# Performance work log

Hardware: AMD Instinct MI355X
Metric: run time of the kernel (lower is better)

## Reference

```python
import jax, jax.numpy as jnp
import numpy as np

N = 4096      # mesh nodes (seq len)
D = 512       # input_dim_nodes / hidden_size
F = 512       # ffn_hidden_size (hidden_dim)
NH = 4        # num_attention_heads
HD = D // NH  # head dim = 128
L = 2         # processor_layers
EPS = 1e-5
SCALE = 1.0 / float(np.sqrt(HD))
NEG = -1e9


def setup_inputs() -> dict:
    key = jax.random.key(0)
    ks = jax.random.split(key, 16)
    nfeat = jax.random.normal(ks[0], (N, D), jnp.float32)
    # sparse graph adjacency mask: True = masked out (TE 'arbitrary' convention)
    mask = jax.random.uniform(ks[1], (N, N)) < 0.99
    idx = jnp.arange(N)
    mask = mask.at[idx, idx].set(False)  # keep self-edges unmasked
    s = 0.02
    p = lambda k, shape: jax.random.normal(k, shape, jnp.float32) * s
    return dict(
        nfeat=nfeat, mask=mask,
        ln1_g=jnp.ones((L, D), jnp.float32), ln1_b=jnp.zeros((L, D), jnp.float32),
        wq=p(ks[2], (L, D, D)), bq=p(ks[3], (L, D)),
        wk=p(ks[4], (L, D, D)), bk=p(ks[5], (L, D)),
        wv=p(ks[6], (L, D, D)), bv=p(ks[7], (L, D)),
        wo=p(ks[8], (L, D, D)), bo=p(ks[9], (L, D)),
        ln2_g=jnp.ones((L, D), jnp.float32), ln2_b=jnp.zeros((L, D), jnp.float32),
        fc1_w=p(ks[10], (L, F, D)), fc1_b=p(ks[11], (L, F)),
        fc2_w=p(ks[12], (L, D, F)), fc2_b=p(ks[13], (L, D)),
    )


def _ln(x, g, b):
    mu = x.mean(-1, keepdims=True)
    var = ((x - mu) ** 2).mean(-1, keepdims=True)
    return (x - mu) * jax.lax.rsqrt(var + EPS) * g + b


def reference(nfeat, mask, ln1_g, ln1_b, wq, bq, wk, bk, wv, bv, wo, bo,
              ln2_g, ln2_b, fc1_w, fc1_b, fc2_w, fc2_b):
    def layer(x, p):
        g1, b1, Wq, Bq, Wk, Bk, Wv, Bv, Wo, Bo, g2, b2, W1, B1, W2, B2 = p
        # --- pre-LN self-attention with arbitrary mask ---
        h = _ln(x, g1, b1)                                  # [N, D]
        q = (h @ Wq.T + Bq).reshape(N, NH, HD)
        k = (h @ Wk.T + Bk).reshape(N, NH, HD)
        v = (h @ Wv.T + Bv).reshape(N, NH, HD)
        scores = jnp.einsum('qhd,khd->hqk', q, k) * SCALE   # [NH, N, N]
        scores = jnp.where(mask[None], NEG, scores)
        attn = jax.nn.softmax(scores, axis=-1)
        o = jnp.einsum('hqk,khd->qhd', attn, v).reshape(N, D)
        x = x + o @ Wo.T + Bo
        # --- pre-LN MLP ---
        h2 = _ln(x, g2, b2)
        m = jax.nn.gelu(h2 @ W1.T + B1, approximate=False) @ W2.T + B2
        return x + m, None

    xs = (ln1_g, ln1_b, wq, bq, wk, bk, wv, bv, wo, bo,
          ln2_g, ln2_b, fc1_w, fc1_b, fc2_w, fc2_b)
    out, _ = jax.lax.scan(layer, nfeat, xs)
    return out
```

## Files before the change

### kernel.cpp

```cpp
#include <hip/hip_runtime.h>
#include <math.h>

#define NN 4096
#define DD 512
#define FF 512
#define CAP 256
#define SCALE 0.08838834764831845f

typedef unsigned short u16;
typedef unsigned char u8;
typedef __attribute__((ext_vector_type(8))) short short8;
typedef __attribute__((ext_vector_type(8))) unsigned short ushort8;
typedef __attribute__((ext_vector_type(4))) unsigned short ushort4v;
typedef __attribute__((ext_vector_type(4))) float floatx4;
typedef __attribute__((ext_vector_type(2))) float f32x2;
typedef _Float16 half8v __attribute__((ext_vector_type(8)));

__device__ __forceinline__ float bf2f(u16 u) {
    union { unsigned int i; float f; } x; x.i = ((unsigned int)u) << 16; return x.f;
}
__device__ __forceinline__ u16 f2bf(float f) {
    union { float f; unsigned int i; } x; x.f = f;
    unsigned int r = (x.i + 0x7FFFu + ((x.i >> 16) & 1u)) >> 16;
    return (u16)r;
}
__device__ __forceinline__ u16 f2h(float f) {
    _Float16 h = (_Float16)f;
    union { _Float16 h; u16 u; } x; x.h = h; return x.u;
}
__device__ __forceinline__ u8 f2fp8(float f) {
    union { _Float16 h; u16 u; } x;
    x.h = (_Float16)(f * 0.00390625f);
    u16 h = x.u;
    h = h + 0x3F + ((h >> 7) & 1);
    return (u8)(((h >> 8) & 0x80) | ((h >> 7) & 0x7f));
}
__device__ __forceinline__ float fp82f_sw(u8 b) {
    union { u16 u; _Float16 h; } x;
    x.u = (u16)(((u16)(b & 0x80) << 8) | ((u16)(b & 0x7f) << 7));
    return (float)x.h * 256.0f;
}
__device__ __forceinline__ void gld_lds16(const void* g, void* l) {
    __builtin_amdgcn_global_load_lds((const __attribute__((address_space(1))) void*)g,
                                     (__attribute__((address_space(3))) void*)l, 16, 0, 0);
}

struct W6 {
    const float* w[6];
    const float* bq; const float* bk; const float* bv;
};
__global__ void setup_kernel(W6 wp, u16* __restrict__ dst, float* __restrict__ bcat,
                             const int* __restrict__ mask, int* __restrict__ idx,
                             int* __restrict__ cnt) {
    __shared__ int c;
    if (blockIdx.x >= 192) {
        int row = blockIdx.x - 192;
        if (threadIdx.x == 0) c = 0;
        __syncthreads();
        const int4* mrow = (const int4*)(mask + (size_t)row * NN);
        for (int j4 = threadIdx.x; j4 < NN / 4; j4 += blockDim.x) {
            int4 m4 = mrow[j4];
            int base = j4 * 4;
            if (m4.x == 0) idx[row * CAP + atomicAdd(&c, 1)] = base;
            if (m4.y == 0) idx[row * CAP + atomicAdd(&c, 1)] = base + 1;
            if (m4.z == 0) idx[row * CAP + atomicAdd(&c, 1)] = base + 2;
            if (m4.w == 0) idx[row * CAP + atomicAdd(&c, 1)] = base + 3;
        }
        __syncthreads();
        if (threadIdx.x == 0) cnt[row] = (c < CAP) ? c : CAP;
        return;
    }
    int region = blockIdx.x >> 4;
    int layer = region / 6, mat = region - layer * 6;
    const float* src = wp.w[mat] + (size_t)layer * (DD * DD);
    u16* d = dst + (size_t)region * (DD * DD);
    int off = (blockIdx.x & 15) * 16384 + threadIdx.x * 4;
#pragma unroll
    for (int i = 0; i < 16; i++) {
        int e = off + i * 1024;
        float4 f = *(const float4*)&src[e];
        ushort4v u;
        u.x = f2bf(f.x); u.y = f2bf(f.y); u.z = f2bf(f.z); u.w = f2bf(f.w);
        *(ushort4v*)&d[e] = u;
    }
    if (blockIdx.x < 2) {
        int l = blockIdx.x;
        for (int it = 0; it < 6; it++) {
            int j = it * 256 + threadIdx.x;
            int m = j >> 9, col = j & 511;
            const float* bp = (m == 0) ? wp.bq : (m == 1) ? wp.bk : wp.bv;
            bcat[l * 1536 + j] = bp[l * DD + col];
        }
    }
}

__global__ void ln_kernel(const float* __restrict__ x, const float* __restrict__ g,
                          const float* __restrict__ b, u16* __restrict__ out) {
    int wave = threadIdx.x >> 6, lane = threadIdx.x & 63;
    int row = blockIdx.x * 4 + wave;
    const float* xr = x + (size_t)row * DD;
    float4 p0 = *(const float4*)&xr[lane * 8];
    float4 p1 = *(const float4*)&xr[lane * 8 + 4];
    float v[8] = {p0.x, p0.y, p0.z, p0.w, p1.x, p1.y, p1.z, p1.w};
    float s = 0.f;
#pragma unroll
    for (int i = 0; i < 8; i++) s += v[i];
#pragma unroll
    for (int off = 32; off; off >>= 1) s += __shfl_xor(s, off);
    float mu = s * (1.0f / DD);
    float vs = 0.f;
#pragma unroll
    for (int i = 0; i < 8; i++) { float d = v[i] - mu; vs += d * d; }
#pragma unroll
    for (int off = 32; off; off >>= 1) vs += __shfl_xor(vs, off);
    float r = rsqrtf(vs * (1.0f / DD) + 1e-5f);
    float4 g0 = *(const float4*)&g[lane * 8];
    float4 g1 = *(const float4*)&g[lane * 8 + 4];
    float4 b0 = *(const float4*)&b[lane * 8];
    float4 b1 = *(const float4*)&b[lane * 8 + 4];
    float ge[8] = {g0.x, g0.y, g0.z, g0.w, g1.x, g1.y, g1.z, g1.w};
    float be[8] = {b0.x, b0.y, b0.z, b0.w, b1.x, b1.y, b1.z, b1.w};
    ushort8 ov;
#pragma unroll
    for (int i = 0; i < 8; i++) ov[i] = f2bf((v[i] - mu) * r * ge[i] + be[i]);
    *(ushort8*)&out[(size_t)row * DD + lane * 8] = ov;
}

__device__ __forceinline__ float gelu_fast(float val) {
    float z = fabsf(val) * 0.70710678118654752f;
    float tt = __builtin_amdgcn_rcpf(fmaf(0.3275911f, z, 1.0f));
    float p = fmaf(1.061405429f, tt, -1.453152027f);
    p = fmaf(p, tt, 1.421413741f);
    p = fmaf(p, tt, -0.284496736f);
    p = fmaf(p, tt, 0.254829592f);
    p = p * tt * __expf(-z * z);
    float er_ = 1.0f - p;
    float sgn = (val < 0.f) ? -er_ : er_;
    return val * 0.5f * (1.0f + sgn);
}


template <int MODE>
__launch_bounds__(256)
__global__ void gemm_bf16(const u16* __restrict__ A, const u16* __restrict__ B,
                          const float* __restrict__ bias, const float* __restrict__ resIn,
                          float* __restrict__ resOut, u16* __restrict__ outB,
                          int M, int Nout, int K) {
    __shared__ u16 As[2 * 64 * 64];
    __shared__ u16 Bs[2 * 64 * 64];
    const int m0 = blockIdx.y * 64, n0 = blockIdx.x * 64;
    const int t = threadIdx.x;
    const int wave = t >> 6, lane = t & 63;
    const int wm = (wave & 1) * 32, wn = (wave >> 1) * 32;
    const int sr = t >> 3;
    const int sc = ((((t & 7) - (t >> 3)) & 7)) * 8;
    const int fr = lane & 15, g0 = lane >> 4;
    const int er = (lane >> 4) * 4, ec = lane & 15;

    floatx4 acc[2][2] = {};
    const u16* ag0 = A + (size_t)(m0 + sr) * K + sc;
    const u16* ag1 = A + (size_t)(m0 + 32 + sr) * K + sc;
    const u16* bg0 = B + (size_t)(n0 + sr) * K + sc;
    const u16* bg1 = B + (size_t)(n0 + 32 + sr) * K + sc;
    u16* as0 = As + t * 8;
    u16* as1 = As + 32 * 64 + t * 8;
    u16* bs0 = Bs + t * 8;
    u16* bs1 = Bs + 32 * 64 + t * 8;

    float rin[16];
    if (MODE == 2) {
#pragma unroll
        for (int i = 0; i < 2; i++)
#pragma unroll
            for (int j = 0; j < 2; j++)
#pragma unroll
                for (int r = 0; r < 4; r++)
                    rin[(i * 2 + j) * 4 + r] =
                        resIn[(size_t)(m0 + wm + 16 * i + er + r) * Nout + (n0 + wn + 16 * j + ec)];
    }

    auto stage = [&](int buf, int k0) {
        int o = buf * 4096;
        gld_lds16(ag0 + k0, as0 + o);
        gld_lds16(ag1 + k0, as1 + o);
        gld_lds16(bg0 + k0, bs0 + o);
        gld_lds16(bg1 + k0, bs1 + o);
    };

    const int NK = K >> 6;
    stage(0, 0);
    int cur = 0;
    for (int kt = 0; kt < NK; kt++) {
        __syncthreads();
        if (kt + 1 < NK) stage(cur ^ 1, (kt + 1) * 64);
        const u16* Ab = As + cur * 4096;
        const u16* Bb = Bs + cur * 4096;
#pragma unroll
        for (int h = 0; h < 2; h++) {
            const int fo = (((h << 2) + g0 + fr) & 7) << 3;
            short8 af[2], bf[2];
#pragma unroll
            for (int i = 0; i < 2; i++) af[i] = *(const short8*)&Ab[(wm + 16 * i + fr) * 64 + fo];
#pragma unroll
            for (int j = 0; j < 2; j++) bf[j] = *(const short8*)&Bb[(wn + 16 * j + fr) * 64 + fo];
#pragma unroll
            for (int i = 0; i < 2; i++)
#pragma unroll
                for (int j = 0; j < 2; j++)
                    acc[i][j] = __builtin_amdgcn_mfma_f32_16x16x32_bf16(af[i], bf[j], acc[i][j], 0, 0, 0);
        }
        cur ^= 1;
    }

#pragma unroll
    for (int i = 0; i < 2; i++) {
#pragma unroll
        for (int j = 0; j < 2; j++) {
            int col = n0 + wn + 16 * j + ec;
            float bsv = bias[col];
#pragma unroll
            for (int r = 0; r < 4; r++) {
                int row = m0 + wm + 16 * i + er + r;
                float val = acc[i][j][r] + bsv;
                if (MODE == 1) val = gelu_fast(val);
                if (MODE == 2) {
                    resOut[(size_t)row * Nout + col] = rin[(i * 2 + j) * 4 + r] + val;
                } else {
                    outB[(size_t)row * Nout + col] = f2bf(val);
                }
            }
        }
    }
}

__launch_bounds__(256)
__global__ void gemm_qkv(const u16* __restrict__ A, const u16* __restrict__ B,
                         const float* __restrict__ bias, u16* __restrict__ qOut,
                         u8* __restrict__ kv8) {
    __shared__ u16 As[2 * 128 * 64];
    __shared__ u16 Bs[2 * 64 * 64];
    const int m0 = blockIdx.y * 128, n0 = blockIdx.x * 64;
    const int t = threadIdx.x;
    const int wave = t >> 6, lane = t & 63;
    const int wm = (wave & 1) * 64, wn = (wave >> 1) * 32;
    const int sr = t >> 3;
    const int sc = ((((t & 7) - (t >> 3)) & 7)) * 8;
    const int fr = lane & 15, g0 = lane >> 4;

    floatx4 acc[4][2] = {};
    const u16* agp[4];
    u16* asp[4];
#pragma unroll
    for (int u = 0; u < 4; u++) {
        agp[u] = A + (size_t)(m0 + 32 * u + sr) * DD + sc;
        asp[u] = As + u * (32 * 64) + t * 8;
    }
    const u16* bg0 = B + (size_t)(n0 + sr) * DD + sc;
    const u16* bg1 = B + (size_t)(n0 + 32 + sr) * DD + sc;
    u16* bs0 = Bs + t * 8;
    u16* bs1 = Bs + 32 * 64 + t * 8;

    auto stage = [&](int buf, int k0) {
        int oa = buf * 8192, ob = buf * 4096;
#pragma unroll
        for (int u = 0; u < 4; u++) gld_lds16(agp[u] + k0, asp[u] + oa);
        gld_lds16(bg0 + k0, bs0 + ob);
        gld_lds16(bg1 + k0, bs1 + ob);
    };

    stage(0, 0);
    int cur = 0;
    for (int kt = 0; kt < 8; kt++) {
        __syncthreads();
        if (kt + 1 < 8) stage(cur ^ 1, (kt + 1) * 64);
        const u16* Ab = As + cur * 8192;
        const u16* Bb = Bs + cur * 4096;
#pragma unroll
        for (int h = 0; h < 2; h++) {
            const int fo = (((h << 2) + g0 + fr) & 7) << 3;
            short8 af[4], bf[2];
#pragma unroll
            for (int i = 0; i < 4; i++) af[i] = *(const short8*)&Ab[(wm + 16 * i + fr) * 64 + fo];
#pragma unroll
            for (int j = 0; j < 2; j++) bf[j] = *(const short8*)&Bb[(wn + 16 * j + fr) * 64 + fo];
#pragma unroll
            for (int i = 0; i < 4; i++)
#pragma unroll
                for (int j = 0; j < 2; j++)
                    acc[i][j] = __builtin_amdgcn_mfma_f32_16x16x32_bf16(af[i], bf[j], acc[i][j], 0, 0, 0);
        }
        cur ^= 1;
    }

    const int er = (lane >> 4) * 4, ec = lane & 15;
    const int bx = blockIdx.x;
#pragma unroll
    for (int j = 0; j < 2; j++) {
        int col = n0 + wn + 16 * j + ec;
        float bsv = bias[col];
#pragma unroll
        for (int i = 0; i < 4; i++) {
#pragma unroll
            for (int r = 0; r < 4; r++) {
                int row = m0 + wm + 16 * i + er + r;
                float val = acc[i][j][r] + bsv;
                if (bx < 8) {
                    qOut[(size_t)row * 512 + col] = f2h(val);
                } else if (bx < 16) {
                    int cc = col - 512;
                    kv8[(size_t)row * 1024 + 16 * (cc >> 3) + (cc & 7)] = f2fp8(val);
                } else {
                    int cc = col - 1024;
                    kv8[(size_t)row * 1024 + 16 * (cc >> 3) + 8 + (cc & 7)] = f2fp8(val);
                }
            }
        }
    }
}

__global__ void sparse_attn(const u16* __restrict__ q, const u8* __restrict__ kv8,
                            const int* __restrict__ idx, const int* __restrict__ cnt,
                            u16* __restrict__ o) {
    int t = threadIdx.x;
    int wave = t >> 6, lane = t & 63;
    int qslot = wave >> 1, half = wave & 1;
    int qi = blockIdx.x * 4 + qslot;
    __shared__ float obuf[4][64][8];
    __shared__ float sbuf[4][64];
    __shared__ int sidx[4][CAP];

    int c = cnt[qi];
    const int* ir = idx + qi * CAP;
    for (int j = t & 127; j < c; j += 128) sidx[qslot][j] = ir[j];

    half8v qv = *(const half8v*)(q + (size_t)qi * 512 + lane * 8);
    float qf[8];
#pragma unroll
    for (int e = 0; e < 8; e++) qf[e] = (float)qv[e];
    __syncthreads();

    float sum = 0.f, oa[8] = {};
    int j = half;
    int4 kv0, kv1;
    {
        int k0i = (j < c) ? sidx[qslot][j] : 0;
        int k1i = (j + 2 < c) ? sidx[qslot][j + 2] : 0;
        kv0 = *(const int4*)(kv8 + (size_t)k0i * 1024 + lane * 16);
        kv1 = *(const int4*)(kv8 + (size_t)k1i * 1024 + lane * 16);
    }
    while (j < c) {
        int4 kvn;
        {
            int kjn = (j + 4 < c) ? sidx[qslot][j + 4] : 0;
            kvn = *(const int4*)(kv8 + (size_t)kjn * 1024 + lane * 16);
        }
        float kd[8], vd[8];
#if __has_builtin(__builtin_amdgcn_cvt_pk_f32_fp8)
        {
            f32x2 p0 = __builtin_amdgcn_cvt_pk_f32_fp8(kv0.x, false);
            f32x2 p1 = __builtin_amdgcn_cvt_pk_f32_fp8(kv0.x, true);
            f32x2 p2 = __builtin_amdgcn_cvt_pk_f32_fp8(kv0.y, false);
            f32x2 p3 = __builtin_amdgcn_cvt_pk_f32_fp8(kv0.y, true);
            kd[0] = p0.x; kd[1] = p0.y; kd[2] = p1.x; kd[3] = p1.y;
            kd[4] = p2.x; kd[5] = p2.y; kd[6] = p3.x; kd[7] = p3.y;
            f32x2 p4 = __builtin_amdgcn_cvt_pk_f32_fp8(kv0.z, false);
            f32x2 p5 = __builtin_amdgcn_cvt_pk_f32_fp8(kv0.z, true);
            f32x2 p6 = __builtin_amdgcn_cvt_pk_f32_fp8(kv0.w, false);
            f32x2 p7 = __builtin_amdgcn_cvt_pk_f32_fp8(kv0.w, true);
            vd[0] = p4.x; vd[1] = p4.y; vd[2] = p5.x; vd[3] = p5.y;
            vd[4] = p6.x; vd[5] = p6.y; vd[6] = p7.x; vd[7] = p7.y;
        }
#else
        {
            const u8* bp = (const u8*)&kv0;
#pragma unroll
            for (int e = 0; e < 8; e++) { kd[e] = fp82f_sw(bp[e]); vd[e] = fp82f_sw(bp[8 + e]); }
        }
#endif
        float d = 0.f;
#pragma unroll
        for (int e = 0; e < 8; e++) d = fmaf(qf[e], kd[e], d);
        d += __shfl_xor(d, 1);
        d += __shfl_xor(d, 2);
        d += __shfl_xor(d, 4);
        d += __shfl_xor(d, 8);
        float p = __expf(d * SCALE);
        sum += p;
#pragma unroll
        for (int e = 0; e < 8; e++) oa[e] = fmaf(p, vd[e], oa[e]);
        kv0 = kv1;
        kv1 = kvn;
        j += 2;
    }

    if (half == 1) {
#pragma unroll
        for (int e = 0; e < 8; e++) obuf[qslot][lane][e] = oa[e];
        sbuf[qslot][lane] = sum;
    }
    __syncthreads();
    if (half == 0) {
        sum += sbuf[qslot][lane];
        float inv = 1.0f / sum;
        ushort8 ov;
#pragma unroll
        for (int e = 0; e < 8; e++) ov[e] = f2bf((oa[e] + obuf[qslot][lane][e]) * inv);
        *(ushort8*)(o + (size_t)qi * 512 + lane * 8) = ov;
    }
}

extern "C" void kernel_launch(void* const* d_in, const int* in_sizes, int n_in,
                              void* d_out, int out_size, void* d_ws, size_t ws_size,
                              hipStream_t stream) {
    const float* nfeat = (const float*)d_in[0];
    const int*   mask  = (const int*)d_in[1];
    const float* ln1_g = (const float*)d_in[2];
    const float* ln1_b = (const float*)d_in[3];
    const float* bo    = (const float*)d_in[11];
    const float* ln2_g = (const float*)d_in[12];
    const float* ln2_b = (const float*)d_in[13];
    const float* fc1_b = (const float*)d_in[15];
    const float* fc2_b = (const float*)d_in[17];

    const size_t ND = (size_t)NN * DD;
    float* x    = (float*)d_ws;
    u16*   h    = (u16*)(x + ND);
    u16*   q    = h + ND;
    u8*    kv8  = (u8*)(q + ND);
    u16*   o    = (u16*)(kv8 + (size_t)NN * 1024);
    u16*   m1   = o + ND;
    u16*   wc   = m1 + ND;
    float* bcat = (float*)(wc + (size_t)12 * DD * DD);
    int*   idx  = (int*)(bcat + 2 * 1536);
    int*   cnt  = idx + (size_t)NN * CAP;

    W6 w6;
    w6.w[0] = (const float*)d_in[4];  w6.w[1] = (const float*)d_in[6];
    w6.w[2] = (const float*)d_in[8];  w6.w[3] = (const float*)d_in[10];
    w6.w[4] = (const float*)d_in[14]; w6.w[5] = (const float*)d_in[16];
    w6.bq = (const float*)d_in[5]; w6.bk = (const float*)d_in[7]; w6.bv = (const float*)d_in[9];
    setup_kernel<<<192 + NN, 256, 0, stream>>>(w6, wc, bcat, mask, idx, cnt);

    const size_t SS = (size_t)DD * DD;
    for (int l = 0; l < 2; l++) {
        size_t bOff = (size_t)l * DD;
        u16* wl = wc + (size_t)l * 6 * SS;
        const float* xin = (l == 0) ? nfeat : x;
        float* fc2_dst = (l == 1) ? (float*)d_out : x;

        ln_kernel<<<NN / 4, 256, 0, stream>>>(xin, ln1_g + bOff, ln1_b + bOff, h);
        gemm_qkv<<<dim3(24, 32), 256, 0, stream>>>(h, wl, bcat + l * 1536, q, kv8);
        sparse_attn<<<NN / 4, 512, 0, stream>>>(q, kv8, idx, cnt, o);
        gemm_bf16<2><<<dim3(8, 64), 256, 0, stream>>>(o, wl + 3 * SS, bo + bOff,
                                                      xin, x, nullptr, NN, DD, DD);
        ln_kernel<<<NN / 4, 256, 0, stream>>>(x, ln2_g + bOff, ln2_b + bOff, h);
        gemm_bf16<1><<<dim3(8, 64), 256, 0, stream>>>(h, wl + 4 * SS, fc1_b + bOff,
                                                      nullptr, nullptr, m1, NN, FF, DD);
        gemm_bf16<2><<<dim3(8, 64), 256, 0, stream>>>(m1, wl + 5 * SS, fc2_b + bOff,
                                                      x, fc2_dst, nullptr, NN, DD, FF);
    }
}
```

Measured before the change: 281.4 us.

## Fold LayerNorm into GEMMs via gamma-scaled weights and per-row stats

```diff
diff --git a/kernel.cpp b/kernel.cpp
--- a/kernel.cpp
+++ b/kernel.cpp
@@ -9,6 +9,7 @@
 
 typedef unsigned short u16;
 typedef unsigned char u8;
+typedef unsigned int u32;
 typedef __attribute__((ext_vector_type(8))) short short8;
 typedef __attribute__((ext_vector_type(8))) unsigned short ushort8;
 typedef __attribute__((ext_vector_type(4))) unsigned short ushort4v;
@@ -16,9 +17,6 @@
 typedef __attribute__((ext_vector_type(2))) float f32x2;
 typedef _Float16 half8v __attribute__((ext_vector_type(8)));
 
-__device__ __forceinline__ float bf2f(u16 u) {
-    union { unsigned int i; float f; } x; x.i = ((unsigned int)u) << 16; return x.f;
-}
 __device__ __forceinline__ u16 f2bf(float f) {
     union { float f; unsigned int i; } x; x.f = f;
     unsigned int r = (x.i + 0x7FFFu + ((x.i >> 16) & 1u)) >> 16;
@@ -43,87 +41,6 @@
 __device__ __forceinline__ void gld_lds16(const void* g, void* l) {
     __builtin_amdgcn_global_load_lds((const __attribute__((address_space(1))) void*)g,
                                      (__attribute__((address_space(3))) void*)l, 16, 0, 0);
-}
-
-struct W6 {
-    const float* w[6];
-    const float* bq; const float* bk; const float* bv;
-};
-__global__ void setup_kernel(W6 wp, u16* __restrict__ dst, float* __restrict__ bcat,
-                             const int* __restrict__ mask, int* __restrict__ idx,
-                             int* __restrict__ cnt) {
-    __shared__ int c;
-    if (blockIdx.x >= 192) {
-        int row = blockIdx.x - 192;
-        if (threadIdx.x == 0) c = 0;
-        __syncthreads();
-        const int4* mrow = (const int4*)(mask + (size_t)row * NN);
-        for (int j4 = threadIdx.x; j4 < NN / 4; j4 += blockDim.x) {
-            int4 m4 = mrow[j4];
-            int base = j4 * 4;
-            if (m4.x == 0) idx[row * CAP + atomicAdd(&c, 1)] = base;
-            if (m4.y == 0) idx[row * CAP + atomicAdd(&c, 1)] = base + 1;
-            if (m4.z == 0) idx[row * CAP + atomicAdd(&c, 1)] = base + 2;
-            if (m4.w == 0) idx[row * CAP + atomicAdd(&c, 1)] = base + 3;
-        }
-        __syncthreads();
-        if (threadIdx.x == 0) cnt[row] = (c < CAP) ? c : CAP;
-        return;
-    }
-    int region = blockIdx.x >> 4;
-    int layer = region / 6, mat = region - layer * 6;
-    const float* src = wp.w[mat] + (size_t)layer * (DD * DD);
-    u16* d = dst + (size_t)region * (DD * DD);
-    int off = (blockIdx.x & 15) * 16384 + threadIdx.x * 4;
-#pragma unroll
-    for (int i = 0; i < 16; i++) {
-        int e = off + i * 1024;
-        float4 f = *(const float4*)&src[e];
-        ushort4v u;
-        u.x = f2bf(f.x); u.y = f2bf(f.y); u.z = f2bf(f.z); u.w = f2bf(f.w);
-        *(ushort4v*)&d[e] = u;
-    }
-    if (blockIdx.x < 2) {
-        int l = blockIdx.x;
-        for (int it = 0; it < 6; it++) {
-            int j = it * 256 + threadIdx.x;
-            int m = j >> 9, col = j & 511;
-            const float* bp = (m == 0) ? wp.bq : (m == 1) ? wp.bk : wp.bv;
-            bcat[l * 1536 + j] = bp[l * DD + col];
-        }
-    }
-}
-
-__global__ void ln_kernel(const float* __restrict__ x, const float* __restrict__ g,
-                          const float* __restrict__ b, u16* __restrict__ out) {
-    int wave = threadIdx.x >> 6, lane = threadIdx.x & 63;
-    int row = blockIdx.x * 4 + wave;
-    const float* xr = x + (size_t)row * DD;
-    float4 p0 = *(const float4*)&xr[lane * 8];
-    float4 p1 = *(const float4*)&xr[lane * 8 + 4];
-    float v[8] = {p0.x, p0.y, p0.z, p0.w, p1.x, p1.y, p1.z, p1.w};
-    float s = 0.f;
-#pragma unroll
-    for (int i = 0; i < 8; i++) s += v[i];
-#pragma unroll
-    for (int off = 32; off; off >>= 1) s += __shfl_xor(s, off);
-    float mu = s * (1.0f / DD);
-    float vs = 0.f;
-#pragma unroll
-    for (int i = 0; i < 8; i++) { float d = v[i] - mu; vs += d * d; }
-#pragma unroll
-    for (int off = 32; off; off >>= 1) vs += __shfl_xor(vs, off);
-    float r = rsqrtf(vs * (1.0f / DD) + 1e-5f);
-    float4 g0 = *(const float4*)&g[lane * 8];
-    float4 g1 = *(const float4*)&g[lane * 8 + 4];
-    float4 b0 = *(const float4*)&b[lane * 8];
-    float4 b1 = *(const float4*)&b[lane * 8 + 4];
-    float ge[8] = {g0.x, g0.y, g0.z, g0.w, g1.x, g1.y, g1.z, g1.w};
-    float be[8] = {b0.x, b0.y, b0.z, b0.w, b1.x, b1.y, b1.z, b1.w};
-    ushort8 ov;
-#pragma unroll
-    for (int i = 0; i < 8; i++) ov[i] = f2bf((v[i] - mu) * r * ge[i] + be[i]);
-    *(ushort8*)&out[(size_t)row * DD + lane * 8] = ov;
 }
 
 __device__ __forceinline__ float gelu_fast(float val) {
@@ -139,15 +56,124 @@
     return val * 0.5f * (1.0f + sgn);
 }
 
-
-template <int MODE>
+struct SP {
+    const float* w[6];
+    const float* bq; const float* bk; const float* bv; const float* fc1_b;
+    const float* ln1_g; const float* ln1_b; const float* ln2_g; const float* ln2_b;
+    const float* nfeat; const int* mask;
+};
+__global__ void setup_kernel(SP sp, u16* __restrict__ wc, float* __restrict__ bc2,
+                             float* __restrict__ c1c, float* __restrict__ st,
+                             u16* __restrict__ xb, int* __restrict__ idx,
+                             int* __restrict__ cnt) {
+    const int bid = blockIdx.x;
+    const int t = threadIdx.x;
+    const int wave = t >> 6, lane = t & 63;
+    if (bid < 192) {
+        int region = bid >> 4;
+        int layer = region / 6, mat = region - layer * 6;
+        const float* src = sp.w[mat] + (size_t)layer * (DD * DD);
+        u16* d = wc + (size_t)region * (DD * DD);
+        int off = (bid & 15) * 16384 + t * 4;
+        int k = (t * 4) & 511;
+        float4 g4 = {1.f, 1.f, 1.f, 1.f};
+        if (mat < 3)      g4 = *(const float4*)&sp.ln1_g[layer * DD + k];
+        else if (mat == 4) g4 = *(const float4*)&sp.ln2_g[layer * DD + k];
+#pragma unroll
+        for (int i = 0; i < 16; i++) {
+            int e = off + i * 1024;
+            float4 f = *(const float4*)&src[e];
+            ushort4v u;
+            u.x = f2bf(f.x * g4.x); u.y = f2bf(f.y * g4.y);
+            u.z = f2bf(f.z * g4.z); u.w = f2bf(f.w * g4.w);
+            *(ushort4v*)&d[e] = u;
+        }
+        if (bid == 2 || bid == 3) {
+            float* z = st + 8192;
+            int base = (bid - 2) * 256 + t;
+#pragma unroll
+            for (int i = 0; i < 48; i++) z[base + i * 512] = 0.0f;
+        }
+        return;
+    }
+    if (bid < 192 + NN) {
+        int row = bid - 192;
+        __shared__ int c;
+        __shared__ float ws[4][2];
+        const float* xr = sp.nfeat + (size_t)row * DD;
+        float2 v2 = *(const float2*)&xr[t * 2];
+        float s1 = v2.x + v2.y, s2 = v2.x * v2.x + v2.y * v2.y;
+#pragma unroll
+        for (int off = 32; off; off >>= 1) { s1 += __shfl_xor(s1, off); s2 += __shfl_xor(s2, off); }
+        if (lane == 0) { ws[wave][0] = s1; ws[wave][1] = s2; }
+        u32 pack = (u32)f2bf(v2.x) | ((u32)f2bf(v2.y) << 16);
+        ((u32*)xb)[row * 256 + t] = pack;
+        if (t == 0) c = 0;
+        __syncthreads();
+        if (t == 0) {
+            float S1 = ws[0][0] + ws[1][0] + ws[2][0] + ws[3][0];
+            float S2 = ws[0][1] + ws[1][1] + ws[2][1] + ws[3][1];
+            st[row * 2] = S1; st[row * 2 + 1] = S2;
+        }
+        const int4* mrow = (const int4*)(sp.mask + (size_t)row * NN);
+        for (int j4 = t; j4 < NN / 4; j4 += blockDim.x) {
+            int4 m4 = mrow[j4];
+            int base = j4 * 4;
+            if (m4.x == 0) idx[row * CAP + atomicAdd(&c, 1)] = base;
+            if (m4.y == 0) idx[row * CAP + atomicAdd(&c, 1)] = base + 1;
+            if (m4.z == 0) idx[row * CAP + atomicAdd(&c, 1)] = base + 2;
+            if (m4.w == 0) idx[row * CAP + atomicAdd(&c, 1)] = base + 3;
+        }
+        __syncthreads();
+        if (t == 0) cnt[row] = (c < CAP) ? c : CAP;
+        return;
+    }
+    {
+        int cb = bid - (192 + NN);
+        for (int pass = 0; pass < 64; pass++) {
+            int colg = cb * 256 + pass * 4 + wave;
+            int l = colg >> 11, j = colg & 2047;
+            const float* W; const float* g; const float* b; float bias;
+            if (j < 1536) {
+                int mat = j >> 9, col = j & 511;
+                W = sp.w[mat] + (size_t)l * DD * DD + (size_t)col * DD;
+                g = sp.ln1_g + l * DD; b = sp.ln1_b + l * DD;
+                bias = (mat == 0 ? sp.bq : mat == 1 ? sp.bk : sp.bv)[l * DD + col];
+            } else {
+                int col = j - 1536;
+                W = sp.w[4] + (size_t)l * DD * DD + (size_t)col * DD;
+                g = sp.ln2_g + l * DD; b = sp.ln2_b + l * DD;
+                bias = sp.fc1_b[l * DD + col];
+            }
+            int k = lane * 8;
+            float4 w0 = *(const float4*)&W[k];
+            float4 w1 = *(const float4*)&W[k + 4];
+            float4 g0 = *(const float4*)&g[k];
+            float4 g1 = *(const float4*)&g[k + 4];
+            float4 b0 = *(const float4*)&b[k];
+            float4 b1 = *(const float4*)&b[k + 4];
+            float c1 = w0.x * g0.x + w0.y * g0.y + w0.z * g0.z + w0.w * g0.w
+                     + w1.x * g1.x + w1.y * g1.y + w1.z * g1.z + w1.w * g1.w;
+            float c2 = w0.x * b0.x + w0.y * b0.y + w0.z * b0.z + w0.w * b0.w
+                     + w1.x * b1.x + w1.y * b1.y + w1.z * b1.z + w1.w * b1.w;
+#pragma unroll
+            for (int off = 32; off; off >>= 1) { c1 += __shfl_xor(c1, off); c2 += __shfl_xor(c2, off); }
+            if (lane == 0) { c1c[colg] = c1; bc2[colg] = bias + c2; }
+        }
+    }
+}
+
+
+template <int MODE, int LNF>
 __launch_bounds__(256)
-__global__ void gemm_bf16(const u16* __restrict__ A, const u16* __restrict__ B,
-                          const float* __restrict__ bias, const float* __restrict__ resIn,
-                          float* __restrict__ resOut, u16* __restrict__ outB,
-                          int M, int Nout, int K) {
-    __shared__ u16 As[2 * 64 * 64];
-    __shared__ u16 Bs[2 * 64 * 64];
+__global__ void gemm_fc(const u16* __restrict__ A, const u16* __restrict__ B,
+                        const float* __restrict__ bias, const float* __restrict__ c1,
+                        const float* __restrict__ stats, const float* __restrict__ resIn,
+                        float* __restrict__ resOut, u16* __restrict__ outB,
+                        u16* __restrict__ xbOut, float* __restrict__ statsOut) {
+    __shared__ __align__(16) u8 smem[16384];
+    u16* As = (u16*)smem;
+    u16* Bs = (u16*)(smem + 8192);
     const int m0 = blockIdx.y * 64, n0 = blockIdx.x * 64;
     const int t = threadIdx.x;
     const int wave = t >> 6, lane = t & 63;
@@ -158,14 +184,10 @@
     const int er = (lane >> 4) * 4, ec = lane & 15;
 
     floatx4 acc[2][2] = {};
-    const u16* ag0 = A + (size_t)(m0 + sr) * K + sc;
-    const u16* ag1 = A + (size_t)(m0 + 32 + sr) * K + sc;
-    const u16* bg0 = B + (size_t)(n0 + sr) * K + sc;
-    const u16* bg1 = B + (size_t)(n0 + 32 + sr) * K + sc;
-    u16* as0 = As + t * 8;
-    u16* as1 = As + 32 * 64 + t * 8;
-    u16* bs0 = Bs + t * 8;
-    u16* bs1 = Bs + 32 * 64 + t * 8;
+    const u16* ag0 = A + (size_t)(m0 + sr) * 512 + sc;
+    const u16* ag1 = A + (size_t)(m0 + 32 + sr) * 512 + sc;
+    const u16* bg0 = B + (size_t)(n0 + sr) * 512 + sc;
+    const u16* bg1 = B + (size_t)(n0 + 32 + sr) * 512 + sc;
 
     float rin[16];
     if (MODE == 2) {
@@ -176,69 +198,103 @@
 #pragma unroll
                 for (int r = 0; r < 4; r++)
                     rin[(i * 2 + j) * 4 + r] =
-                        resIn[(size_t)(m0 + wm + 16 * i + er + r) * Nout + (n0 + wn + 16 * j + ec)];
-    }
-
-    auto stage = [&](int buf, int k0) {
-        int o = buf * 4096;
-        gld_lds16(ag0 + k0, as0 + o);
-        gld_lds16(ag1 + k0, as1 + o);
-        gld_lds16(bg0 + k0, bs0 + o);
-        gld_lds16(bg1 + k0, bs1 + o);
-    };
-
-    const int NK = K >> 6;
-    stage(0, 0);
-    int cur = 0;
-    for (int kt = 0; kt < NK; kt++) {
-        __syncthreads();
-        if (kt + 1 < NK) stage(cur ^ 1, (kt + 1) * 64);
-        const u16* Ab = As + cur * 4096;
-        const u16* Bb = Bs + cur * 4096;
+                        resIn[(size_t)(m0 + wm + 16 * i + er + r) * 512 + (n0 + wn + 16 * j + ec)];
+    }
+    float ar[2][4], br[2][4];
+    if (LNF) {
+#pragma unroll
+        for (int i = 0; i < 2; i++) {
+            int r0 = m0 + wm + 16 * i + er;
+#pragma unroll
+            for (int r = 0; r < 4; r++) {
+                f32x2 s = *(const f32x2*)&stats[(r0 + r) * 2];
+                float m = s.x * (1.0f / DD);
+                float rr = rsqrtf(s.y * (1.0f / DD) - m * m + 1e-5f);
+                ar[i][r] = rr; br[i][r] = -rr * m;
+            }
+        }
+    }
+
+    for (int k0 = 0; k0 < 512; k0 += 64) {
+        __syncthreads();
+        gld_lds16(ag0 + k0, As + t * 8);
+        gld_lds16(ag1 + k0, As + 2048 + t * 8);
+        gld_lds16(bg0 + k0, Bs + t * 8);
+        gld_lds16(bg1 + k0, Bs + 2048 + t * 8);
+        __syncthreads();
 #pragma unroll
         for (int h = 0; h < 2; h++) {
             const int fo = (((h << 2) + g0 + fr) & 7) << 3;
             short8 af[2], bf[2];
 #pragma unroll
-            for (int i = 0; i < 2; i++) af[i] = *(const short8*)&Ab[(wm + 16 * i + fr) * 64 + fo];
-#pragma unroll
-            for (int j = 0; j < 2; j++) bf[j] = *(const short8*)&Bb[(wn + 16 * j + fr) * 64 + fo];
+            for (int i = 0; i < 2; i++) af[i] = *(const short8*)&As[(wm + 16 * i + fr) * 64 + fo];
+#pragma unroll
+            for (int j = 0; j < 2; j++) bf[j] = *(const short8*)&Bs[(wn + 16 * j + fr) * 64 + fo];
 #pragma unroll
             for (int i = 0; i < 2; i++)
 #pragma unroll
                 for (int j = 0; j < 2; j++)
                     acc[i][j] = __builtin_amdgcn_mfma_f32_16x16x32_bf16(af[i], bf[j], acc[i][j], 0, 0, 0);
         }
-        cur ^= 1;
-    }
-
-#pragma unroll
-    for (int i = 0; i < 2; i++) {
-#pragma unroll
-        for (int j = 0; j < 2; j++) {
-            int col = n0 + wn + 16 * j + ec;
-            float bsv = bias[col];
+    }
+
+    float outv[16];
+#pragma unroll
+    for (int j = 0; j < 2; j++) {
+        int col = n0 + wn + 16 * j + ec;
+        float bsv = bias[col];
+        float c1v = LNF ? c1[col] : 0.f;
+#pragma unroll
+        for (int i = 0; i < 2; i++) {
 #pragma unroll
             for (int r = 0; r < 4; r++) {
                 int row = m0 + wm + 16 * i + er + r;
-                float val = acc[i][j][r] + bsv;
-                if (MODE == 1) val = gelu_fast(val);
-                if (MODE == 2) {
-                    resOut[(size_t)row * Nout + col] = rin[(i * 2 + j) * 4 + r] + val;
+                float val;
+                if (LNF) val = fmaf(ar[i][r], acc[i][j][r], fmaf(br[i][r], c1v, bsv));
+                else     val = acc[i][j][r] + bsv;
+                if (MODE == 1) {
+                    outB[(size_t)row * 512 + col] = f2bf(gelu_fast(val));
                 } else {
-                    outB[(size_t)row * Nout + col] = f2bf(val);
+                    float ov = rin[(i * 2 + j) * 4 + r] + val;
+                    outv[(i * 2 + j) * 4 + r] = ov;
+                    resOut[(size_t)row * 512 + col] = ov;
+                    if (xbOut) xbOut[(size_t)row * 512 + col] = f2bf(ov);
                 }
             }
         }
     }
+
+    if (MODE == 2 && statsOut) {
+        __syncthreads();
+        float* Ls = (float*)smem;
+#pragma unroll
+        for (int i = 0; i < 2; i++)
+#pragma unroll
+            for (int j = 0; j < 2; j++)
+#pragma unroll
+                for (int r = 0; r < 4; r++)
+                    Ls[(wm + 16 * i + er + r) * 64 + (wn + 16 * j + ec)] = outv[(i * 2 + j) * 4 + r];
+        __syncthreads();
+        if (t < 64) {
+            float s1 = 0.f, s2 = 0.f;
+            for (int c0 = 0; c0 < 64; c0++) {
+                int cc = (c0 + t) & 63;
+                float v = Ls[t * 64 + cc];
+                s1 += v; s2 += v * v;
+            }
+            atomicAdd(&statsOut[(size_t)(m0 + t) * 2], s1);
+            atomicAdd(&statsOut[(size_t)(m0 + t) * 2 + 1], s2);
+        }
+    }
 }
 
 __launch_bounds__(256)
 __global__ void gemm_qkv(const u16* __restrict__ A, const u16* __restrict__ B,
-                         const float* __restrict__ bias, u16* __restrict__ qOut,
+                         const float* __restrict__ bias, const float* __restrict__ c1,
+                         const float* __restrict__ stats, u16* __restrict__ qOut,
                          u8* __restrict__ kv8) {
-    __shared__ u16 As[2 * 128 * 64];
-    __shared__ u16 Bs[2 * 64 * 64];
+    __shared__ u16 As[128 * 64];
+    __shared__ u16 Bs[64 * 64];
     const int m0 = blockIdx.y * 128, n0 = blockIdx.x * 64;
     const int t = threadIdx.x;
     const int wave = t >> 6, lane = t & 63;
@@ -246,6 +302,7 @@
     const int sr = t >> 3;
     const int sc = ((((t & 7) - (t >> 3)) & 7)) * 8;
     const int fr = lane & 15, g0 = lane >> 4;
+    const int er = (lane >> 4) * 4, ec = lane & 15;
 
     floatx4 acc[4][2] = {};
     const u16* agp[4];
@@ -257,53 +314,55 @@
     }
     const u16* bg0 = B + (size_t)(n0 + sr) * DD + sc;
     const u16* bg1 = B + (size_t)(n0 + 32 + sr) * DD + sc;
-    u16* bs0 = Bs + t * 8;
-    u16* bs1 = Bs + 32 * 64 + t * 8;
-
-    auto stage = [&](int buf, int k0) {
-        int oa = buf * 8192, ob = buf * 4096;
-#pragma unroll
-        for (int u = 0; u < 4; u++) gld_lds16(agp[u] + k0, asp[u] + oa);
-        gld_lds16(bg0 + k0, bs0 + ob);
-        gld_lds16(bg1 + k0, bs1 + ob);
-    };
-
-    stage(0, 0);
-    int cur = 0;
-    for (int kt = 0; kt < 8; kt++) {
-        __syncthreads();
-        if (kt + 1 < 8) stage(cur ^ 1, (kt + 1) * 64);
-        const u16* Ab = As + cur * 8192;
-        const u16* Bb = Bs + cur * 4096;
+
+    float ar[4][4], br[4][4];
+#pragma unroll
+    for (int i = 0; i < 4; i++) {
+        int r0 = m0 + wm + 16 * i + er;
+#pragma unroll
+        for (int r = 0; r < 4; r++) {
+            f32x2 s = *(const f32x2*)&stats[(r0 + r) * 2];
+            float m = s.x * (1.0f / DD);
+            float rr = rsqrtf(s.y * (1.0f / DD) - m * m + 1e-5f);
+            ar[i][r] = rr; br[i][r] = -rr * m;
+        }
+    }
+
+    for (int k0 = 0; k0 < DD; k0 += 64) {
+        __syncthreads();
+#pragma unroll
+        for (int u = 0; u < 4; u++) gld_lds16(agp[u] + k0, asp[u]);
+        gld_lds16(bg0 + k0, Bs + t * 8);
+        gld_lds16(bg1 + k0, Bs + 2048 + t * 8);
+        __syncthreads();
 #pragma unroll
         for (int h = 0; h < 2; h++) {
             const int fo = (((h << 2) + g0 + fr) & 7) << 3;
             short8 af[4], bf[2];
 #pragma unroll
-            for (int i = 0; i < 4; i++) af[i] = *(const short8*)&Ab[(wm + 16 * i + fr) * 64 + fo];
-#pragma unroll
-            for (int j = 0; j < 2; j++) bf[j] = *(const short8*)&Bb[(wn + 16 * j + fr) * 64 + fo];
+            for (int i = 0; i < 4; i++) af[i] = *(const short8*)&As[(wm + 16 * i + fr) * 64 + fo];
+#pragma unroll
+            for (int j = 0; j < 2; j++) bf[j] = *(const short8*)&Bs[(wn + 16 * j + fr) * 64 + fo];
 #pragma unroll
             for (int i = 0; i < 4; i++)
 #pragma unroll
                 for (int j = 0; j < 2; j++)
                     acc[i][j] = __builtin_amdgcn_mfma_f32_16x16x32_bf16(af[i], bf[j], acc[i][j], 0, 0, 0);
         }
-        cur ^= 1;
-    }
-
-    const int er = (lane >> 4) * 4, ec = lane & 15;
+    }
+
     const int bx = blockIdx.x;
 #pragma unroll
     for (int j = 0; j < 2; j++) {
         int col = n0 + wn + 16 * j + ec;
         float bsv = bias[col];
+        float c1v = c1[col];
 #pragma unroll
         for (int i = 0; i < 4; i++) {
 #pragma unroll
             for (int r = 0; r < 4; r++) {
                 int row = m0 + wm + 16 * i + er + r;
-                float val = acc[i][j][r] + bsv;
+                float val = fmaf(ar[i][r], acc[i][j][r], fmaf(br[i][r], c1v, bsv));
                 if (bx < 8) {
                     qOut[(size_t)row * 512 + col] = f2h(val);
                 } else if (bx < 16) {
@@ -413,50 +472,58 @@
                               void* d_out, int out_size, void* d_ws, size_t ws_size,
                               hipStream_t stream) {
     const float* nfeat = (const float*)d_in[0];
-    const int*   mask  = (const int*)d_in[1];
-    const float* ln1_g = (const float*)d_in[2];
-    const float* ln1_b = (const float*)d_in[3];
     const float* bo    = (const float*)d_in[11];
-    const float* ln2_g = (const float*)d_in[12];
-    const float* ln2_b = (const float*)d_in[13];
-    const float* fc1_b = (const float*)d_in[15];
     const float* fc2_b = (const float*)d_in[17];
 
     const size_t ND = (size_t)NN * DD;
+    const size_t SS = (size_t)DD * DD;
     float* x    = (float*)d_ws;
-    u16*   h    = (u16*)(x + ND);
-    u16*   q    = h + ND;
+    u16*   xb   = (u16*)(x + ND);
+    u16*   q    = xb + ND;
     u8*    kv8  = (u8*)(q + ND);
     u16*   o    = (u16*)(kv8 + (size_t)NN * 1024);
     u16*   m1   = o + ND;
     u16*   wc   = m1 + ND;
-    float* bcat = (float*)(wc + (size_t)12 * DD * DD);
-    int*   idx  = (int*)(bcat + 2 * 1536);
+    float* bc2  = (float*)(wc + 12 * SS);
+    float* c1c  = bc2 + 2 * 2048;
+    float* st   = c1c + 2 * 2048;
+    int*   idx  = (int*)(st + 4 * 8192);
     int*   cnt  = idx + (size_t)NN * CAP;
 
-    W6 w6;
-    w6.w[0] = (const float*)d_in[4];  w6.w[1] = (const float*)d_in[6];
-    w6.w[2] = (const float*)d_in[8];  w6.w[3] = (const float*)d_in[10];
-    w6.w[4] = (const float*)d_in[14]; w6.w[5] = (const float*)d_in[16];
-    w6.bq = (const float*)d_in[5]; w6.bk = (const float*)d_in[7]; w6.bv = (const float*)d_in[9];
-    setup_kernel<<<192 + NN, 256, 0, stream>>>(w6, wc, bcat, mask, idx, cnt);
-
-    const size_t SS = (size_t)DD * DD;
+    SP sp;
+    sp.w[0] = (const float*)d_in[4];  sp.bq = (const float*)d_in[5];
+    sp.w[1] = (const float*)d_in[6];  sp.bk = (const float*)d_in[7];
+    sp.w[2] = (const float*)d_in[8];  sp.bv = (const float*)d_in[9];
+    sp.w[3] = (const float*)d_in[10];
+    sp.w[4] = (const float*)d_in[14]; sp.fc1_b = (const float*)d_in[15];
+    sp.w[5] = (const float*)d_in[16];
+    sp.ln1_g = (const float*)d_in[2];  sp.ln1_b = (const float*)d_in[3];
+    sp.ln2_g = (const float*)d_in[12]; sp.ln2_b = (const float*)d_in[13];
+    sp.nfeat = nfeat; sp.mask = (const int*)d_in[1];
+
+    setup_kernel<<<192 + NN + 16, 256, 0, stream>>>(sp, wc, bc2, c1c, st, xb, idx, cnt);
+
     for (int l = 0; l < 2; l++) {
         size_t bOff = (size_t)l * DD;
         u16* wl = wc + (size_t)l * 6 * SS;
         const float* xin = (l == 0) ? nfeat : x;
         float* fc2_dst = (l == 1) ? (float*)d_out : x;
-
-        ln_kernel<<<NN / 4, 256, 0, stream>>>(xin, ln1_g + bOff, ln1_b + bOff, h);
-        gemm_qkv<<<dim3(24, 32), 256, 0, stream>>>(h, wl, bcat + l * 1536, q, kv8);
+        float* st_ln1 = st + (l == 0 ? 0 : 2) * 8192;
+        float* st_ln2 = st + (l == 0 ? 1 : 3) * 8192;
+
+        gemm_qkv<<<dim3(24, 32), 256, 0, stream>>>(xb, wl, bc2 + l * 2048, c1c + l * 2048,
+                                                   st_ln1, q, kv8);
         sparse_attn<<<NN / 4, 512, 0, stream>>>(q, kv8, idx, cnt, o);
-        gemm_bf16<2><<<dim3(8, 64), 256, 0, stream>>>(o, wl + 3 * SS, bo + bOff,
-                                                      xin, x, nullptr, NN, DD, DD);
-        ln_kernel<<<NN / 4, 256, 0, stream>>>(x, ln2_g + bOff, ln2_b + bOff, h);
-        gemm_bf16<1><<<dim3(8, 64), 256, 0, stream>>>(h, wl + 4 * SS, fc1_b + bOff,
-                                                      nullptr, nullptr, m1, NN, FF, DD);
-        gemm_bf16<2><<<dim3(8, 64), 256, 0, stream>>>(m1, wl + 5 * SS, fc2_b + bOff,
-                                                      x, fc2_dst, nullptr, NN, DD, FF);
-    }
-}
+        gemm_fc<2, 0><<<dim3(8, 64), 256, 0, stream>>>(o, wl + 3 * SS, bo + bOff, nullptr,
+                                                       nullptr, xin, x, nullptr, xb, st_ln2);
+        gemm_fc<1, 1><<<dim3(8, 64), 256, 0, stream>>>(xb, wl + 4 * SS,
+                                                       bc2 + l * 2048 + 1536,
+                                                       c1c + l * 2048 + 1536,
+                                                       st_ln2, nullptr, nullptr, m1,
+                                                       nullptr, nullptr);
+        gemm_fc<2, 0><<<dim3(8, 64), 256, 0, stream>>>(m1, wl + 5 * SS, fc2_b + bOff, nullptr,
+                                                       nullptr, x, fc2_dst, nullptr,
+                                                       (l == 0) ? xb : nullptr,
+                                                       (l == 0) ? (st + 2 * 8192) : nullptr);
+    }
+}
```

Result: slower. 325.7 us (+15.8%).
